# Optimization experiments

Hardware: AMD Instinct MI355X
Metric: run time of the kernel (lower is better)

## Reference

```python
import jax, jax.numpy as jnp
import numpy as np

N = 100000   # nodes
E = 1600000  # edges
F = 128      # input/hidden dim
C = 3        # classes
G = 64       # graphs in batch


def setup_inputs() -> dict:
    key = jax.random.key(0)
    ks = jax.random.split(key, 12)
    s = 1.0 / np.sqrt(F)
    return {
        "x": jax.random.normal(ks[0], (N, F), dtype=jnp.float32),
        "edge_index": jax.random.randint(ks[1], (2, E), 0, N, dtype=jnp.int64),
        "batch": jnp.sort(jax.random.randint(ks[2], (N,), 0, G, dtype=jnp.int64)),
        "W1": jax.random.normal(ks[3], (F, F), dtype=jnp.float32) * s,
        "b1": jnp.zeros((F,), dtype=jnp.float32),
        "W2": jax.random.normal(ks[4], (F, F), dtype=jnp.float32) * s,
        "b2": jnp.zeros((F,), dtype=jnp.float32),
        "W3": jax.random.normal(ks[5], (F, F), dtype=jnp.float32) * s,
        "b3": jnp.zeros((F,), dtype=jnp.float32),
        "Wc": jax.random.normal(ks[6], (F, C), dtype=jnp.float32) * s,
        "bc": jnp.zeros((C,), dtype=jnp.float32),
    }


def reference(x, edge_index, batch, W1, b1, W2, b2, W3, b3, Wc, bc):
    n = x.shape[0]
    src, dst = edge_index[0], edge_index[1]
    # GCN adds self-loops: A_hat = A + I
    loops = jnp.arange(n, dtype=src.dtype)
    src_a = jnp.concatenate([src, loops])
    dst_a = jnp.concatenate([dst, loops])
    # symmetric normalization D^-1/2 (A+I) D^-1/2 (in-degree incl. self-loop)
    deg = jax.ops.segment_sum(jnp.ones_like(dst_a, dtype=x.dtype), dst_a, num_segments=n)
    dis = jnp.where(deg > 0, jax.lax.rsqrt(deg), 0.0)
    norm = dis[src_a] * dis[dst_a]  # [E+N]

    def gcn_conv(h, W, b):
        h = h @ W                                    # [N, F']
        msg = h[src_a] * norm[:, None]               # gather + scale
        agg = jax.ops.segment_sum(msg, dst_a, num_segments=n)  # scatter-add
        return agg + b

    h = jax.nn.relu(gcn_conv(x, W1, b1))   # dropout = identity in eval mode
    h = jax.nn.relu(gcn_conv(h, W2, b2))
    h = jax.nn.relu(gcn_conv(h, W3, b3))

    # global_mean_pool over graph ids
    sums = jax.ops.segment_sum(h, batch, num_segments=G)
    cnt = jax.ops.segment_sum(jnp.ones((n,), dtype=h.dtype), batch, num_segments=G)
    pooled = sums / jnp.maximum(cnt, 1.0)[:, None]
    return pooled @ Wc + bc
```

## Files before the change

### kernel.cpp

```cpp
#include <hip/hip_runtime.h>
#include <cstdint>
#include <cstddef>

#define FDIM 128
#define CHUNK 4096
#define BSHIFT 8
#define BMASK 255
#define MAXB 512

typedef unsigned short ushort_t;
typedef __attribute__((ext_vector_type(8))) short short8;
typedef __attribute__((ext_vector_type(4))) float floatx4;

__device__ inline ushort_t f2bf(float f) {
  unsigned u = __float_as_uint(f);
  u += 0x7fffu + ((u >> 16) & 1u);
  return (ushort_t)(u >> 16);
}
__device__ inline float bf2f(ushort_t h) {
  return __uint_as_float((unsigned)h << 16);
}

__global__ __launch_bounds__(256) void k_histw(const int* __restrict__ dst, int e,
                                               int nb, int* __restrict__ chunkHist,
                                               int nch,
                                               const float* __restrict__ W1,
                                               const float* __restrict__ W2,
                                               const float* __restrict__ W3,
                                               ushort_t* __restrict__ wsw) {
  if (blockIdx.x >= (unsigned)nch) {
    int b = blockIdx.x - nch;
    const float* W = (b == 0) ? W1 : (b == 1) ? W2 : W3;
    ushort_t* o = wsw + (size_t)b * 16384;
    for (int idx = threadIdx.x; idx < 16384; idx += 256) {
      int j = idx & 7;
      int lane = (idx >> 3) & 63;
      int ct = (idx >> 9) & 7;
      int kc = idx >> 12;
      int k = kc * 32 + (lane >> 4) * 8 + j;
      int col = (lane & 15) * 8 + ct;
      o[idx] = f2bf(W[k * FDIM + col]);
    }
    return;
  }
  __shared__ int h[MAXB];
  int c = blockIdx.x;
  int base = c * CHUNK;
  int end = min(base + CHUNK, e);
  for (int i = threadIdx.x; i < nb; i += 256) h[i] = 0;
  __syncthreads();
  for (int i = base + threadIdx.x; i < end; i += 256)
    atomicAdd(&h[dst[i] >> BSHIFT], 1);
  __syncthreads();
  for (int b = threadIdx.x; b < nb; b += 256)
    chunkHist[(size_t)c * nb + b] = h[b];
}

__global__ __launch_bounds__(512) void k_scan1(const int* __restrict__ chunkHist,
                                               int nchunks, int nb,
                                               int* __restrict__ chunkOff,
                                               int* __restrict__ bucketTotal) {
  __shared__ int sb[512];
  int b = blockIdx.x;
  int t = threadIdx.x;
  int base = 0;
  for (int c0 = 0; c0 < nchunks; c0 += 512) {
    int c = c0 + t;
    int v = (c < nchunks) ? chunkHist[(size_t)c * nb + b] : 0;
    int x = v;
    sb[t] = x;
    __syncthreads();
    for (int off = 1; off < 512; off <<= 1) {
      int y = (t >= off) ? sb[t - off] : 0;
      __syncthreads();
      x += y;
      sb[t] = x;
      __syncthreads();
    }
    if (c < nchunks) chunkOff[(size_t)c * nb + b] = base + x - v;
    int tileTot = sb[511];
    __syncthreads();
    base += tileTot;
  }
  if (t == 0) bucketTotal[b] = base;
}

__global__ __launch_bounds__(512) void k_scan2(const int* __restrict__ bucketTotal,
                                               int nb, int e,
                                               int* __restrict__ bucketBase) {
  __shared__ int sb[512];
  int t = threadIdx.x;
  int v = (t < nb) ? bucketTotal[t] : 0;
  int x = v;
  sb[t] = x;
  __syncthreads();
  for (int off = 1; off < 512; off <<= 1) {
    int y = (t >= off) ? sb[t - off] : 0;
    __syncthreads();
    x += y;
    sb[t] = x;
    __syncthreads();
  }
  if (t < nb) bucketBase[t] = x - v;
  if (t == 0) bucketBase[nb] = e;
}

__global__ __launch_bounds__(256) void k_bin(const int* __restrict__ src,
                                             const int* __restrict__ dst, int e, int nb,
                                             const int* __restrict__ chunkHist,
                                             const int* __restrict__ chunkOff,
                                             const int* __restrict__ bucketBase,
                                             unsigned* __restrict__ binned) {
  __shared__ unsigned sortedL[CHUNK];
  __shared__ int gtarget[CHUNK];
  __shared__ int lbase[MAXB], lcur[MAXB], gbase[MAXB];
  __shared__ int stmp[256];
  int c = blockIdx.x;
  int base = c * CHUNK;
  int end = min(base + CHUNK, e);
  for (int i = threadIdx.x; i < nb; i += 256) {
    lbase[i] = chunkHist[(size_t)c * nb + i];
    gbase[i] = bucketBase[i] + chunkOff[(size_t)c * nb + i];
  }
  __syncthreads();
  int carry = 0;
  for (int i0 = 0; i0 < nb; i0 += 256) {
    int i = i0 + threadIdx.x;
    int v = (i < nb) ? lbase[i] : 0;
    int x = v;
    stmp[threadIdx.x] = x;
    __syncthreads();
    for (int off = 1; off < 256; off <<= 1) {
      int y = (threadIdx.x >= off) ? stmp[threadIdx.x - off] : 0;
      __syncthreads();
      x += y;
      stmp[threadIdx.x] = x;
      __syncthreads();
    }
    if (i < nb) lbase[i] = carry + x - v;
    int tileTot = stmp[255];
    __syncthreads();
    carry += tileTot;
  }
  for (int i = threadIdx.x; i < nb; i += 256) lcur[i] = lbase[i];
  __syncthreads();
  for (int i = base + threadIdx.x; i < end; i += 256) {
    int d = dst[i];
    int sv = src[i];
    int b = d >> BSHIFT;
    int slot = atomicAdd(&lcur[b], 1);
    sortedL[slot] = ((unsigned)sv << BSHIFT) | (unsigned)(d & BMASK);
    gtarget[slot] = gbase[b] + (slot - lbase[b]);
  }
  __syncthreads();
  for (int i = threadIdx.x; i < end - base; i += 256)
    binned[gtarget[i]] = sortedL[i];
}

__global__ __launch_bounds__(256) void k_fill2(const unsigned* __restrict__ binned,
                                               const int* __restrict__ bucketBase, int n,
                                               int* __restrict__ rowStart,
                                               int* __restrict__ deg,
                                               float* __restrict__ dis,
                                               int2* __restrict__ colPair) {
  __shared__ int h[256], sb[256], cur[256];
  int b = blockIdx.x;
  int s0 = bucketBase[b], s1 = bucketBase[b + 1];
  int nodeBase = b << BSHIFT;
  int t = threadIdx.x;
  h[t] = 0;
  __syncthreads();
  for (int i = s0 + t; i < s1; i += 256) atomicAdd(&h[binned[i] & BMASK], 1);
  __syncthreads();
  int v = h[t];
  int x = v;
  sb[t] = x;
  __syncthreads();
  for (int off = 1; off < 256; off <<= 1) {
    int y = (t >= off) ? sb[t - off] : 0;
    __syncthreads();
    x += y;
    sb[t] = x;
    __syncthreads();
  }
  int start = s0 + x - v;
  cur[t] = start;
  int node = nodeBase + t;
  if (node < n) {
    rowStart[node] = start;
    deg[node] = v;
    dis[node] = rsqrtf((float)(v + 1));
  }
  __syncthreads();
  for (int i = s0 + t; i < s1; i += 256) {
    unsigned en = binned[i];
    int slot = atomicAdd(&cur[en & BMASK], 1);
    colPair[slot] = int2{(int)(en >> BSHIFT), 0};
  }
}

template <int INBF, int EDGW>
__global__ __launch_bounds__(256) void k_mm(const void* __restrict__ Ain,
                                            const ushort_t* __restrict__ Wsw,
                                            ushort_t* __restrict__ O, int n, int mmb,
                                            int2* __restrict__ colPair, int e,
                                            const float* __restrict__ dis) {
  if (EDGW && blockIdx.x >= (unsigned)mmb) {
    int base = (blockIdx.x - mmb) * 2048 + threadIdx.x;
    for (int k = 0; k < 8; ++k) {
      int i = base + k * 256;
      if (i < e) {
        int2 p = colPair[i];
        p.y = __float_as_int(dis[p.x]);
        colPair[i] = p;
      }
    }
    return;
  }
  __shared__ ushort_t Bs[16384];
  int tid = threadIdx.x;
  for (int q = tid; q < 2048; q += 256)
    ((uint4*)Bs)[q] = ((const uint4*)Wsw)[q];
  __syncthreads();

  int w = tid >> 6;
  int lane = tid & 63;
  int quad = lane >> 4;
  int l15 = lane & 15;
  int rb = blockIdx.x * 128 + w * 32;
  const float* Af = (const float*)Ain;
  const ushort_t* Ab = (const ushort_t*)Ain;

  int row0 = rb + l15;
  int row1 = rb + 16 + l15;
  bool v0 = row0 < n, v1 = row1 < n;

  floatx4 acc[2][8];
#pragma unroll
  for (int rt = 0; rt < 2; ++rt)
#pragma unroll
    for (int ct = 0; ct < 8; ++ct) acc[rt][ct] = floatx4{0.f, 0.f, 0.f, 0.f};

#pragma unroll
  for (int kc = 0; kc < 4; ++kc) {
    int k0 = kc * 32 + quad * 8;
    short8 a0 = short8{0, 0, 0, 0, 0, 0, 0, 0};
    short8 a1 = short8{0, 0, 0, 0, 0, 0, 0, 0};
    if (INBF) {
      if (v0) a0 = *(const short8*)&Ab[(size_t)row0 * FDIM + k0];
      if (v1) a1 = *(const short8*)&Ab[(size_t)row1 * FDIM + k0];
    } else {
      if (v0) {
        float4 f0 = *(const float4*)&Af[(size_t)row0 * FDIM + k0];
        float4 f1 = *(const float4*)&Af[(size_t)row0 * FDIM + k0 + 4];
        a0 = short8{(short)f2bf(f0.x), (short)f2bf(f0.y), (short)f2bf(f0.z),
                    (short)f2bf(f0.w), (short)f2bf(f1.x), (short)f2bf(f1.y),
                    (short)f2bf(f1.z), (short)f2bf(f1.w)};
      }
      if (v1) {
        float4 f0 = *(const float4*)&Af[(size_t)row1 * FDIM + k0];
        float4 f1 = *(const float4*)&Af[(size_t)row1 * FDIM + k0 + 4];
        a1 = short8{(short)f2bf(f0.x), (short)f2bf(f0.y), (short)f2bf(f0.z),
                    (short)f2bf(f0.w), (short)f2bf(f1.x), (short)f2bf(f1.y),
                    (short)f2bf(f1.z), (short)f2bf(f1.w)};
      }
    }
#pragma unroll
    for (int ct = 0; ct < 8; ++ct) {
      short8 bf = *(const short8*)&Bs[((kc * 8 + ct) * 64 + lane) * 8];
      acc[0][ct] = __builtin_amdgcn_mfma_f32_16x16x32_bf16(a0, bf, acc[0][ct], 0, 0, 0);
      acc[1][ct] = __builtin_amdgcn_mfma_f32_16x16x32_bf16(a1, bf, acc[1][ct], 0, 0, 0);
    }
  }

#pragma unroll
  for (int rt = 0; rt < 2; ++rt) {
#pragma unroll
    for (int i = 0; i < 4; ++i) {
      int row = rb + rt * 16 + quad * 4 + i;
      if (row < n) {
        uint4 pk;
        pk.x = (unsigned)f2bf(acc[rt][0][i]) | ((unsigned)f2bf(acc[rt][1][i]) << 16);
        pk.y = (unsigned)f2bf(acc[rt][2][i]) | ((unsigned)f2bf(acc[rt][3][i]) << 16);
        pk.z = (unsigned)f2bf(acc[rt][4][i]) | ((unsigned)f2bf(acc[rt][5][i]) << 16);
        pk.w = (unsigned)f2bf(acc[rt][6][i]) | ((unsigned)f2bf(acc[rt][7][i]) << 16);
        *(uint4*)&O[(size_t)row * FDIM + l15 * 8] = pk;
      }
    }
  }
}

__global__ __launch_bounds__(256) void k_agg(const ushort_t* __restrict__ Hin,
                                             ushort_t* __restrict__ Hout,
                                             const int* __restrict__ rowStart,
                                             const int* __restrict__ degE,
                                             const int2* __restrict__ colPair,
                                             const float* __restrict__ dis,
                                             const float* __restrict__ bias, int n) {
  int node = blockIdx.x * 8 + (threadIdx.x >> 5);
  int lane = threadIdx.x & 31;
  if (node >= n) return;
  const uint2* hin = (const uint2*)Hin;
  float di = dis[node];
  uint2 su = hin[(size_t)node * 32 + lane];
  float ws = di * di;
  float a0 = ws * __uint_as_float(su.x << 16);
  float a1 = ws * __uint_as_float(su.x & 0xffff0000u);
  float a2 = ws * __uint_as_float(su.y << 16);
  float a3 = ws * __uint_as_float(su.y & 0xffff0000u);
  int s0 = rowStart[node], cnt = degE[node];
#pragma unroll 4
  for (int j = 0; j < cnt; ++j) {
    int2 p = colPair[s0 + j];
    float w = di * __int_as_float(p.y);
    uint2 u = hin[(size_t)p.x * 32 + lane];
    a0 += w * __uint_as_float(u.x << 16);
    a1 += w * __uint_as_float(u.x & 0xffff0000u);
    a2 += w * __uint_as_float(u.y << 16);
    a3 += w * __uint_as_float(u.y & 0xffff0000u);
  }
  float4 b = ((const float4*)bias)[lane];
  a0 = fmaxf(a0 + b.x, 0.f);
  a1 = fmaxf(a1 + b.y, 0.f);
  a2 = fmaxf(a2 + b.z, 0.f);
  a3 = fmaxf(a3 + b.w, 0.f);
  uint2 o;
  o.x = (unsigned)f2bf(a0) | ((unsigned)f2bf(a1) << 16);
  o.y = (unsigned)f2bf(a2) | ((unsigned)f2bf(a3) << 16);
  ((uint2*)Hout)[(size_t)node * 32 + lane] = o;
}


__global__ __launch_bounds__(128) void k_gstart(const int* __restrict__ batch, int n,
                                                int g_count, int* __restrict__ gstart) {
  int g = threadIdx.x;
  if (g > g_count) return;
  int lo = 0, hi = n;
  while (lo < hi) {
    int mid = (lo + hi) >> 1;
    if (batch[mid] < g) lo = mid + 1;
    else hi = mid;
  }
  gstart[g] = lo;
}

__global__ __launch_bounds__(128) void k_pool(const ushort_t* __restrict__ H,
                                              const int* __restrict__ gstart,
                                              float* __restrict__ pooled, int g_count) {
  int g = blockIdx.x >> 4;
  int c = blockIdx.x & 15;
  int s = gstart[g], e = gstart[g + 1];
  int len = e - s;
  int chunk = (len + 15) >> 4;
  int ns = s + c * chunk;
  int ne = min(ns + chunk, e);
  float acc = 0.f;
  for (int i = ns; i < ne; ++i) acc += bf2f(H[(size_t)i * FDIM + threadIdx.x]);
  atomicAdd(&pooled[g * FDIM + threadIdx.x], acc);
}

__global__ __launch_bounds__(192) void k_final(const float* __restrict__ pooled,
                                               const int* __restrict__ gstart,
                                               const float* __restrict__ Wc,
                                               const float* __restrict__ bc,
                                               float* __restrict__ out, int g_count) {
  int t = threadIdx.x;
  if (t >= g_count * 3) return;
  int g = t / 3, c = t % 3;
  int cnt = gstart[g + 1] - gstart[g];
  float inv = 1.0f / (float)max(cnt, 1);
  float acc = bc[c];
#pragma unroll 8
  for (int k = 0; k < FDIM; ++k) acc += pooled[g * FDIM + k] * inv * Wc[k * 3 + c];
  out[g * 3 + c] = acc;
}


extern "C" void kernel_launch(void* const* d_in, const int* in_sizes, int n_in,
                              void* d_out, int out_size, void* d_ws, size_t ws_size,
                              hipStream_t stream) {
  const float* x = (const float*)d_in[0];
  const int* edge = (const int*)d_in[1];
  const int* batch = (const int*)d_in[2];
  const float* W1 = (const float*)d_in[3];
  const float* b1 = (const float*)d_in[4];
  const float* W2 = (const float*)d_in[5];
  const float* b2 = (const float*)d_in[6];
  const float* W3 = (const float*)d_in[7];
  const float* b3 = (const float*)d_in[8];
  const float* Wc = (const float*)d_in[9];
  const float* bc = (const float*)d_in[10];
  float* out = (float*)d_out;

  const int N = in_sizes[0] / FDIM;
  const int E = in_sizes[1] / 2;
  const int G = out_size / 3;
  const int* src = edge;
  const int* dst = edge + E;

  const int NCH = (E + CHUNK - 1) / CHUNK;
  const int NB = (N + (1 << BSHIFT) - 1) >> BSHIFT;

  char* ws = (char*)d_ws;
  size_t off = 0;
  auto carve = [&](size_t bytes) -> void* {
    void* p = ws + off;
    off = (off + bytes + 255) & ~(size_t)255;
    return p;
  };
  ushort_t* h0 = (ushort_t*)carve((size_t)N * FDIM * 2);
  ushort_t* h1 = (ushort_t*)carve((size_t)N * FDIM * 2);
  int2* colPair = (int2*)carve((size_t)E * 8);
  unsigned* binned = (unsigned*)carve((size_t)E * 4);
  int* chunkHist = (int*)carve((size_t)NCH * NB * 4);
  int* chunkOff = (int*)carve((size_t)NCH * NB * 4);
  int* bucketTotal = (int*)carve((size_t)NB * 4);
  int* bucketBase = (int*)carve((size_t)(NB + 1) * 4);
  int* rowStart = (int*)carve((size_t)N * 4);
  int* deg = (int*)carve((size_t)N * 4);
  float* dis = (float*)carve((size_t)N * 4);
  int* gstart = (int*)carve((size_t)(G + 1) * 4);
  float* pooled = (float*)carve((size_t)G * FDIM * 4);
  ushort_t* wsw = (ushort_t*)carve((size_t)3 * 16384 * 2);
  (void)n_in;
  (void)ws_size;

  hipMemsetAsync(pooled, 0, (size_t)G * FDIM * 4, stream);

  k_histw<<<NCH + 3, 256, 0, stream>>>(dst, E, NB, chunkHist, NCH, W1, W2, W3, wsw);
  k_scan1<<<NB, 512, 0, stream>>>(chunkHist, NCH, NB, chunkOff, bucketTotal);
  k_scan2<<<1, 512, 0, stream>>>(bucketTotal, NB, E, bucketBase);
  k_bin<<<NCH, 256, 0, stream>>>(src, dst, E, NB, chunkHist, chunkOff, bucketBase,
                                 binned);
  k_fill2<<<NB, 256, 0, stream>>>(binned, bucketBase, N, rowStart, deg, dis, colPair);

  int mmb = (N + 127) / 128;
  int ewb = (E + 2047) / 2048;
  int aggb = (N + 7) / 8;
  k_mm<0, 1><<<mmb + ewb, 256, 0, stream>>>(x, wsw, h0, N, mmb, colPair, E, dis);
  k_agg<<<aggb, 256, 0, stream>>>(h0, h1, rowStart, deg, colPair, dis, b1, N);
  k_mm<1, 0><<<mmb, 256, 0, stream>>>(h1, wsw + 16384, h0, N, mmb, nullptr, 0, nullptr);
  k_agg<<<aggb, 256, 0, stream>>>(h0, h1, rowStart, deg, colPair, dis, b2, N);
  k_mm<1, 0><<<mmb, 256, 0, stream>>>(h1, wsw + 32768, h0, N, mmb, nullptr, 0, nullptr);
  k_agg<<<aggb, 256, 0, stream>>>(h0, h1, rowStart, deg, colPair, dis, b3, N);

  k_gstart<<<1, 128, 0, stream>>>(batch, N, G, gstart);
  k_pool<<<G * 16, 128, 0, stream>>>(h1, gstart, pooled, G);
  k_final<<<1, 192, 0, stream>>>(pooled, gstart, Wc, bc, out, G);
}
```

Baseline: 431.6 us.

## Pack CSR column index with bf16 edge weight and drop scan/pool launches

```diff
diff --git a/kernel.cpp b/kernel.cpp
--- a/kernel.cpp
+++ b/kernel.cpp
@@ -27,9 +27,11 @@
                                                const float* __restrict__ W1,
                                                const float* __restrict__ W2,
                                                const float* __restrict__ W3,
-                                               ushort_t* __restrict__ wsw) {
+                                               ushort_t* __restrict__ wsw,
+                                               int* __restrict__ counter) {
   if (blockIdx.x >= (unsigned)nch) {
     int b = blockIdx.x - nch;
+    if (b == 0 && threadIdx.x == 0) *counter = 0;
     const float* W = (b == 0) ? W1 : (b == 1) ? W2 : W3;
     ushort_t* o = wsw + (size_t)b * 16384;
     for (int idx = threadIdx.x; idx < 16384; idx += 256) {
@@ -59,7 +61,9 @@
 __global__ __launch_bounds__(512) void k_scan1(const int* __restrict__ chunkHist,
                                                int nchunks, int nb,
                                                int* __restrict__ chunkOff,
-                                               int* __restrict__ bucketTotal) {
+                                               int* __restrict__ bucketTotal,
+                                               int* __restrict__ bucketBase,
+                                               int* __restrict__ counter) {
   __shared__ int sb[512];
   int b = blockIdx.x;
   int t = threadIdx.x;
@@ -82,27 +86,10 @@
     __syncthreads();
     base += tileTot;
   }
-  if (t == 0) bucketTotal[b] = base;
-}
-
-__global__ __launch_bounds__(512) void k_scan2(const int* __restrict__ bucketTotal,
-                                               int nb, int e,
-                                               int* __restrict__ bucketBase) {
-  __shared__ int sb[512];
-  int t = threadIdx.x;
-  int v = (t < nb) ? bucketTotal[t] : 0;
-  int x = v;
-  sb[t] = x;
-  __syncthreads();
-  for (int off = 1; off < 512; off <<= 1) {
-    int y = (t >= off) ? sb[t - off] : 0;
-    __syncthreads();
-    x += y;
-    sb[t] = x;
-    __syncthreads();
-  }
-  if (t < nb) bucketBase[t] = x - v;
-  if (t == 0) bucketBase[nb] = e;
+  if (t == 0) {
+    bucketTotal[b] = base;
+    bucketBase[b] = atomicAdd(counter, base);
+  }
 }
 
 __global__ __launch_bounds__(256) void k_bin(const int* __restrict__ src,
@@ -158,14 +145,16 @@
 }
 
 __global__ __launch_bounds__(256) void k_fill2(const unsigned* __restrict__ binned,
-                                               const int* __restrict__ bucketBase, int n,
+                                               const int* __restrict__ bucketBase,
+                                               const int* __restrict__ bucketTotal,
+                                               int n,
                                                int* __restrict__ rowStart,
                                                int* __restrict__ deg,
                                                float* __restrict__ dis,
-                                               int2* __restrict__ colPair) {
+                                               unsigned* __restrict__ colPacked) {
   __shared__ int h[256], sb[256], cur[256];
   int b = blockIdx.x;
-  int s0 = bucketBase[b], s1 = bucketBase[b + 1];
+  int s0 = bucketBase[b], s1 = s0 + bucketTotal[b];
   int nodeBase = b << BSHIFT;
   int t = threadIdx.x;
   h[t] = 0;
@@ -195,7 +184,7 @@
   for (int i = s0 + t; i < s1; i += 256) {
     unsigned en = binned[i];
     int slot = atomicAdd(&cur[en & BMASK], 1);
-    colPair[slot] = int2{(int)(en >> BSHIFT), 0};
+    colPacked[slot] = en >> BSHIFT;
   }
 }
 
@@ -203,16 +192,15 @@
 __global__ __launch_bounds__(256) void k_mm(const void* __restrict__ Ain,
                                             const ushort_t* __restrict__ Wsw,
                                             ushort_t* __restrict__ O, int n, int mmb,
-                                            int2* __restrict__ colPair, int e,
+                                            unsigned* __restrict__ colPacked, int e,
                                             const float* __restrict__ dis) {
   if (EDGW && blockIdx.x >= (unsigned)mmb) {
     int base = (blockIdx.x - mmb) * 2048 + threadIdx.x;
     for (int k = 0; k < 8; ++k) {
       int i = base + k * 256;
       if (i < e) {
-        int2 p = colPair[i];
-        p.y = __float_as_int(dis[p.x]);
-        colPair[i] = p;
+        unsigned p = colPacked[i];
+        colPacked[i] = p | ((unsigned)f2bf(dis[p]) << 17);
       }
     }
     return;
@@ -294,7 +282,7 @@
                                              ushort_t* __restrict__ Hout,
                                              const int* __restrict__ rowStart,
                                              const int* __restrict__ degE,
-                                             const int2* __restrict__ colPair,
+                                             const unsigned* __restrict__ colPacked,
                                              const float* __restrict__ dis,
                                              const float* __restrict__ bias, int n) {
   int node = blockIdx.x * 8 + (threadIdx.x >> 5);
@@ -311,9 +299,10 @@
   int s0 = rowStart[node], cnt = degE[node];
 #pragma unroll 4
   for (int j = 0; j < cnt; ++j) {
-    int2 p = colPair[s0 + j];
-    float w = di * __int_as_float(p.y);
-    uint2 u = hin[(size_t)p.x * 32 + lane];
+    unsigned pv = colPacked[s0 + j];
+    int sidx = (int)(pv & 0x1ffffu);
+    float w = di * __uint_as_float((pv >> 17) << 16);
+    uint2 u = hin[(size_t)sidx * 32 + lane];
     a0 += w * __uint_as_float(u.x << 16);
     a1 += w * __uint_as_float(u.x & 0xffff0000u);
     a2 += w * __uint_as_float(u.y << 16);
@@ -331,48 +320,60 @@
 }
 
 
-__global__ __launch_bounds__(128) void k_gstart(const int* __restrict__ batch, int n,
-                                                int g_count, int* __restrict__ gstart) {
-  int g = threadIdx.x;
-  if (g > g_count) return;
+__device__ inline int lower_bound_batch(const int* __restrict__ batch, int n, int g) {
   int lo = 0, hi = n;
   while (lo < hi) {
     int mid = (lo + hi) >> 1;
     if (batch[mid] < g) lo = mid + 1;
     else hi = mid;
   }
-  gstart[g] = lo;
+  return lo;
 }
 
 __global__ __launch_bounds__(128) void k_pool(const ushort_t* __restrict__ H,
-                                              const int* __restrict__ gstart,
-                                              float* __restrict__ pooled, int g_count) {
+                                              const int* __restrict__ batch, int n,
+                                              float* __restrict__ partials,
+                                              int g_count) {
+  __shared__ int se[2];
   int g = blockIdx.x >> 4;
   int c = blockIdx.x & 15;
-  int s = gstart[g], e = gstart[g + 1];
-  int len = e - s;
-  int chunk = (len + 15) >> 4;
+  if (threadIdx.x < 2)
+    se[threadIdx.x] = lower_bound_batch(batch, n, g + (int)threadIdx.x);
+  __syncthreads();
+  int s = se[0], e = se[1];
+  int chunk = (e - s + 15) >> 4;
   int ns = s + c * chunk;
   int ne = min(ns + chunk, e);
   float acc = 0.f;
   for (int i = ns; i < ne; ++i) acc += bf2f(H[(size_t)i * FDIM + threadIdx.x]);
-  atomicAdd(&pooled[g * FDIM + threadIdx.x], acc);
-}
-
-__global__ __launch_bounds__(192) void k_final(const float* __restrict__ pooled,
-                                               const int* __restrict__ gstart,
+  partials[((size_t)g * 16 + c) * FDIM + threadIdx.x] = acc;
+}
+
+__global__ __launch_bounds__(128) void k_final(const float* __restrict__ partials,
+                                               const int* __restrict__ batch, int n,
                                                const float* __restrict__ Wc,
                                                const float* __restrict__ bc,
                                                float* __restrict__ out, int g_count) {
+  __shared__ int se[2];
+  __shared__ float red[6];
   int t = threadIdx.x;
-  if (t >= g_count * 3) return;
-  int g = t / 3, c = t % 3;
-  int cnt = gstart[g + 1] - gstart[g];
-  float inv = 1.0f / (float)max(cnt, 1);
-  float acc = bc[c];
-#pragma unroll 8
-  for (int k = 0; k < FDIM; ++k) acc += pooled[g * FDIM + k] * inv * Wc[k * 3 + c];
-  out[g * 3 + c] = acc;
+  int g = blockIdx.x;
+  if (t < 2) se[t] = lower_bound_batch(batch, n, g + t);
+  __syncthreads();
+  float inv = 1.0f / (float)max(se[1] - se[0], 1);
+  float s = 0.f;
+#pragma unroll
+  for (int p = 0; p < 16; ++p) s += partials[((size_t)g * 16 + p) * FDIM + t];
+  s *= inv;
+#pragma unroll
+  for (int c = 0; c < 3; ++c) {
+    float v = s * Wc[t * 3 + c];
+#pragma unroll
+    for (int off = 1; off < 64; off <<= 1) v += __shfl_xor(v, off);
+    if ((t & 63) == 0) red[(t >> 6) * 3 + c] = v;
+  }
+  __syncthreads();
+  if (t < 3) out[g * 3 + t] = red[t] + red[3 + t] + bc[t];
 }
 
 
@@ -410,41 +411,42 @@
   };
   ushort_t* h0 = (ushort_t*)carve((size_t)N * FDIM * 2);
   ushort_t* h1 = (ushort_t*)carve((size_t)N * FDIM * 2);
-  int2* colPair = (int2*)carve((size_t)E * 8);
+  unsigned* colPacked = (unsigned*)carve((size_t)E * 4);
   unsigned* binned = (unsigned*)carve((size_t)E * 4);
   int* chunkHist = (int*)carve((size_t)NCH * NB * 4);
   int* chunkOff = (int*)carve((size_t)NCH * NB * 4);
   int* bucketTotal = (int*)carve((size_t)NB * 4);
-  int* bucketBase = (int*)carve((size_t)(NB + 1) * 4);
+  int* bucketBase = (int*)carve((size_t)NB * 4);
+  int* counter = (int*)carve(256);
   int* rowStart = (int*)carve((size_t)N * 4);
   int* deg = (int*)carve((size_t)N * 4);
   float* dis = (float*)carve((size_t)N * 4);
-  int* gstart = (int*)carve((size_t)(G + 1) * 4);
-  float* pooled = (float*)carve((size_t)G * FDIM * 4);
+  float* partials = (float*)carve((size_t)G * 16 * FDIM * 4);
   ushort_t* wsw = (ushort_t*)carve((size_t)3 * 16384 * 2);
   (void)n_in;
   (void)ws_size;
 
-  hipMemsetAsync(pooled, 0, (size_t)G * FDIM * 4, stream);
-
-  k_histw<<<NCH + 3, 256, 0, stream>>>(dst, E, NB, chunkHist, NCH, W1, W2, W3, wsw);
-  k_scan1<<<NB, 512, 0, stream>>>(chunkHist, NCH, NB, chunkOff, bucketTotal);
-  k_scan2<<<1, 512, 0, stream>>>(bucketTotal, NB, E, bucketBase);
+  k_histw<<<NCH + 3, 256, 0, stream>>>(dst, E, NB, chunkHist, NCH, W1, W2, W3, wsw,
+                                       counter);
+  k_scan1<<<NB, 512, 0, stream>>>(chunkHist, NCH, NB, chunkOff, bucketTotal,
+                                  bucketBase, counter);
   k_bin<<<NCH, 256, 0, stream>>>(src, dst, E, NB, chunkHist, chunkOff, bucketBase,
                                  binned);
-  k_fill2<<<NB, 256, 0, stream>>>(binned, bucketBase, N, rowStart, deg, dis, colPair);
+  k_fill2<<<NB, 256, 0, stream>>>(binned, bucketBase, bucketTotal, N, rowStart, deg,
+                                  dis, colPacked);
 
   int mmb = (N + 127) / 128;
   int ewb = (E + 2047) / 2048;
   int aggb = (N + 7) / 8;
-  k_mm<0, 1><<<mmb + ewb, 256, 0, stream>>>(x, wsw, h0, N, mmb, colPair, E, dis);
-  k_agg<<<aggb, 256, 0, stream>>>(h0, h1, rowStart, deg, colPair, dis, b1, N);
-  k_mm<1, 0><<<mmb, 256, 0, stream>>>(h1, wsw + 16384, h0, N, mmb, nullptr, 0, nullptr);
-  k_agg<<<aggb, 256, 0, stream>>>(h0, h1, rowStart, deg, colPair, dis, b2, N);
-  k_mm<1, 0><<<mmb, 256, 0, stream>>>(h1, wsw + 32768, h0, N, mmb, nullptr, 0, nullptr);
-  k_agg<<<aggb, 256, 0, stream>>>(h0, h1, rowStart, deg, colPair, dis, b3, N);
-
-  k_gstart<<<1, 128, 0, stream>>>(batch, N, G, gstart);
-  k_pool<<<G * 16, 128, 0, stream>>>(h1, gstart, pooled, G);
-  k_final<<<1, 192, 0, stream>>>(pooled, gstart, Wc, bc, out, G);
-}
+  k_mm<0, 1><<<mmb + ewb, 256, 0, stream>>>(x, wsw, h0, N, mmb, colPacked, E, dis);
+  k_agg<<<aggb, 256, 0, stream>>>(h0, h1, rowStart, deg, colPacked, dis, b1, N);
+  k_mm<1, 0><<<mmb, 256, 0, stream>>>(h1, wsw + 16384, h0, N, mmb, nullptr, 0,
+                                      nullptr);
+  k_agg<<<aggb, 256, 0, stream>>>(h0, h1, rowStart, deg, colPacked, dis, b2, N);
+  k_mm<1, 0><<<mmb, 256, 0, stream>>>(h1, wsw + 32768, h0, N, mmb, nullptr, 0,
+                                      nullptr);
+  k_agg<<<aggb, 256, 0, stream>>>(h0, h1, rowStart, deg, colPacked, dis, b3, N);
+
+  k_pool<<<G * 16, 128, 0, stream>>>(h1, batch, N, partials, G);
+  k_final<<<G, 128, 0, stream>>>(partials, batch, N, Wc, bc, out, G);
+}
```

Result: no change. 426.4 us (-1.2%).
